# Performance work log

Measured on AMD Instinct MI355X. Metric: run time of the kernel, lower is better.

The kernel has to match this reference:

```python
import jax, jax.numpy as jnp
import numpy as np

N_NODES = 50000
N_EDGES = 600000
D = 128
NEG_SLOPE = 0.2


def _gat_conv(x, src, dst, W, a_src, a_dst, b):
    # x: [N, D]; src/dst: [E'] (self-loops included); PyG GATConv, heads=1
    h = x @ W                               # [N, D]
    alpha_s = h @ a_src                     # [N]
    alpha_d = h @ a_dst                     # [N]
    e = alpha_s[src] + alpha_d[dst]         # [E'] raw scores per edge j->i
    e = jnp.where(e > 0, e, NEG_SLOPE * e)  # LeakyReLU(0.2)
    # segment softmax over incoming edges of each dst node
    m = jax.ops.segment_max(e, dst, num_segments=N_NODES)
    ex = jnp.exp(e - m[dst])
    denom = jax.ops.segment_sum(ex, dst, num_segments=N_NODES)
    alpha = ex / denom[dst]                 # [E']
    out = jax.ops.segment_sum(alpha[:, None] * h[src], dst, num_segments=N_NODES)
    return out + b


def setup_inputs() -> dict:
    key = jax.random.key(0)
    ks = jax.random.split(key, 10)
    scale = 1.0 / np.sqrt(D)
    x = jax.random.normal(ks[0], (N_NODES, D), dtype=jnp.float32)
    edge_index = jax.random.randint(ks[1], (2, N_EDGES), 0, N_NODES, dtype=jnp.int64)
    params = {}
    for i, base in ((1, 2), (2, 6)):
        params[f"W{i}"] = jax.random.normal(ks[base], (D, D), dtype=jnp.float32) * scale
        params[f"a_src{i}"] = jax.random.normal(ks[base + 1], (D,), dtype=jnp.float32) * scale
        params[f"a_dst{i}"] = jax.random.normal(ks[base + 2], (D,), dtype=jnp.float32) * scale
        params[f"b{i}"] = jnp.zeros((D,), dtype=jnp.float32)
    return {"x": x, "edge_index": edge_index, **params}


def reference(x, edge_index, W1, a_src1, a_dst1, b1, W2, a_src2, a_dst2, b2):
    # add self-loops (PyG GATConv default add_self_loops=True)
    loops = jnp.arange(N_NODES, dtype=edge_index.dtype)
    src = jnp.concatenate([edge_index[0], loops])
    dst = jnp.concatenate([edge_index[1], loops])
    h = _gat_conv(x, src, dst, W1, a_src1, a_dst1, b1)
    h = jax.nn.relu(h)  # BasicGNN act between layers, none after last
    out = _gat_conv(h, src, dst, W2, a_src2, a_dst2, b2)
    return out
```

## Files before the change

### kernel.cpp

```cpp
#include <hip/hip_runtime.h>
#include <hip/hip_bf16.h>

#define D 128
#define NEG_SLOPE 0.2f
#define AGG_CHUNK 128
#define CHUNKB 4096

typedef short bf16x8 __attribute__((ext_vector_type(8)));
typedef unsigned short ushort8 __attribute__((ext_vector_type(8)));
typedef float f32x4 __attribute__((ext_vector_type(4)));

__device__ inline unsigned short bfbits(float f) {
  __hip_bfloat16 b = __float2bfloat16(f);
  return *(unsigned short*)&b;
}

__device__ inline float2 bf2_to_f2(unsigned v) {
  return make_float2(__uint_as_float(v << 16), __uint_as_float(v & 0xffff0000u));
}


template <bool RELU, bool BF16IN>
__device__ __forceinline__ void gemm_body(ushort* Wt, int tile,
                                          const void* __restrict__ in,
                                          const float* __restrict__ W,
                                          const float* __restrict__ a_s,
                                          const float* __restrict__ a_d,
                                          ushort* __restrict__ hb,
                                          float* __restrict__ as_out,
                                          float* __restrict__ ad_out, int N) {
  int tid = threadIdx.x;
  for (int u = tid; u < 2048; u += 256) {
    int kp = u >> 5, cg = u & 31;
    int k = kp * 2;
    float4 w0 = *(const float4*)(W + (size_t)k * D + cg * 4);
    float4 w1 = *(const float4*)(W + (size_t)(k + 1) * D + cg * 4);
    float v0[4] = {w0.x, w0.y, w0.z, w0.w};
    float v1[4] = {w1.x, w1.y, w1.z, w1.w};
    #pragma unroll
    for (int i = 0; i < 4; ++i) {
      int c = cg * 4 + i;
      unsigned word = (unsigned)bfbits(v0[i]) | ((unsigned)bfbits(v1[i]) << 16);
      int byte = c * 256 + ((k * 2) ^ ((c & 7) << 4));
      *(unsigned*)((char*)Wt + byte) = word;
    }
  }
  __syncthreads();

  int wave = tid >> 6, lane = tid & 63;
  int lrow = lane & 15, lgrp = lane >> 4;
  int r0 = tile * 128 + wave * 32;
  int rowA[2];
  rowA[0] = min(r0 + lrow, N - 1);
  rowA[1] = min(r0 + 16 + lrow, N - 1);

  f32x4 acc[2][8];
  #pragma unroll
  for (int t = 0; t < 2; ++t)
    #pragma unroll
    for (int nt = 0; nt < 8; ++nt) acc[t][nt] = (f32x4){0.f, 0.f, 0.f, 0.f};

  #pragma unroll
  for (int ks = 0; ks < 4; ++ks) {
    bf16x8 af[2];
    #pragma unroll
    for (int t = 0; t < 2; ++t) {
      if (BF16IN) {
        const ushort* arow = (const ushort*)in + (size_t)rowA[t] * D;
        ushort8 u = *(const ushort8*)(arow + ks * 32 + lgrp * 8);
        if (RELU) {
          #pragma unroll
          for (int j = 0; j < 8; ++j) u[j] = (u[j] & 0x8000u) ? 0 : u[j];
        }
        #pragma unroll
        for (int j = 0; j < 8; ++j) af[t][j] = (short)u[j];
      } else {
        const float* arow = (const float*)in + (size_t)rowA[t] * D;
        float4 a0 = *(const float4*)(arow + ks * 32 + lgrp * 8);
        float4 a1 = *(const float4*)(arow + ks * 32 + lgrp * 8 + 4);
        if (RELU) {
          a0.x = fmaxf(a0.x, 0.f); a0.y = fmaxf(a0.y, 0.f);
          a0.z = fmaxf(a0.z, 0.f); a0.w = fmaxf(a0.w, 0.f);
          a1.x = fmaxf(a1.x, 0.f); a1.y = fmaxf(a1.y, 0.f);
          a1.w = fmaxf(a1.w, 0.f); a1.z = fmaxf(a1.z, 0.f);
        }
        af[t][0] = (short)bfbits(a0.x); af[t][1] = (short)bfbits(a0.y);
        af[t][2] = (short)bfbits(a0.z); af[t][3] = (short)bfbits(a0.w);
        af[t][4] = (short)bfbits(a1.x); af[t][5] = (short)bfbits(a1.y);
        af[t][6] = (short)bfbits(a1.z); af[t][7] = (short)bfbits(a1.w);
      }
    }
    #pragma unroll
    for (int nt = 0; nt < 8; ++nt) {
      int c = nt * 16 + lrow;
      int kb = (ks * 64 + lgrp * 16) ^ ((c & 7) << 4);
      bf16x8 bfr = *(const bf16x8*)((const char*)Wt + c * 256 + kb);
      acc[0][nt] = __builtin_amdgcn_mfma_f32_16x16x32_bf16(af[0], bfr, acc[0][nt], 0, 0, 0);
      acc[1][nt] = __builtin_amdgcn_mfma_f32_16x16x32_bf16(af[1], bfr, acc[1][nt], 0, 0, 0);
    }
  }

  float ps[2][4] = {{0.f,0.f,0.f,0.f},{0.f,0.f,0.f,0.f}};
  float pd[2][4] = {{0.f,0.f,0.f,0.f},{0.f,0.f,0.f,0.f}};
  #pragma unroll
  for (int nt = 0; nt < 8; ++nt) {
    float asc = a_s[nt * 16 + lrow];
    float adc = a_d[nt * 16 + lrow];
    #pragma unroll
    for (int t = 0; t < 2; ++t) {
      #pragma unroll
      for (int r = 0; r < 4; ++r) {
        float v = acc[t][nt][r];
        ps[t][r] += v * asc;
        pd[t][r] += v * adc;
        int row = r0 + t * 16 + lgrp * 4 + r;
        if (row < N) hb[(size_t)row * D + nt * 16 + lrow] = bfbits(v);
      }
    }
  }
  #pragma unroll
  for (int mk = 1; mk < 16; mk <<= 1) {
    #pragma unroll
    for (int t = 0; t < 2; ++t)
      #pragma unroll
      for (int r = 0; r < 4; ++r) {
        ps[t][r] += __shfl_xor(ps[t][r], mk);
        pd[t][r] += __shfl_xor(pd[t][r], mk);
      }
  }
  if (lrow == 0) {
    #pragma unroll
    for (int t = 0; t < 2; ++t)
      #pragma unroll
      for (int r = 0; r < 4; ++r) {
        int row = r0 + t * 16 + lgrp * 4 + r;
        if (row < N) { as_out[row] = ps[t][r]; ad_out[row] = pd[t][r]; }
      }
  }
}

__global__ __launch_bounds__(256) void count_gemm_kernel(const int* __restrict__ ei,
                                                         int* __restrict__ coarse,
                                                         int E, int total, int nbkt, int nblk,
                                                         const float* __restrict__ in,
                                                         const float* __restrict__ W,
                                                         const float* __restrict__ a_s,
                                                         const float* __restrict__ a_d,
                                                         ushort* __restrict__ hb,
                                                         float* __restrict__ as_out,
                                                         float* __restrict__ ad_out, int N) {
  if ((int)blockIdx.x < nblk) {
    __shared__ int hist[256];
    for (int i = threadIdx.x; i < nbkt; i += 256) hist[i] = 0;
    __syncthreads();
    int base = blockIdx.x * CHUNKB;
    int end = min(base + CHUNKB, total);
    for (int e = base + threadIdx.x; e < end; e += 256) {
      int dst = (e < E) ? ei[E + e] : (e - E);
      atomicAdd(&hist[dst >> 8], 1);
    }
    __syncthreads();
    for (int i = threadIdx.x; i < nbkt; i += 256)
      coarse[(size_t)i * nblk + blockIdx.x] = hist[i];
  } else {
    __shared__ ushort Wt[D * D];
    gemm_body<false, false>(Wt, blockIdx.x - nblk, in, W, a_s, a_d, hb, as_out, ad_out, N);
  }
}

__global__ __launch_bounds__(256) void gemm_bf16_kernel(const ushort* __restrict__ in,
                                                        const float* __restrict__ W,
                                                        const float* __restrict__ a_s,
                                                        const float* __restrict__ a_d,
                                                        ushort* __restrict__ hb,
                                                        float* __restrict__ as_out,
                                                        float* __restrict__ ad_out, int N) {
  __shared__ ushort Wt[D * D];
  gemm_body<true, true>(Wt, blockIdx.x, in, W, a_s, a_d, hb, as_out, ad_out, N);
}


__global__ __launch_bounds__(256) void scan_all_kernel(const int* __restrict__ in,
                                                       int* __restrict__ out, int n) {
  __shared__ int wsA[4];
  __shared__ int wsB[4];
  int b = blockIdx.x;
  int tid = threadIdx.x;
  int lane = tid & 63, wid = tid >> 6;

  int pre = 0;
  for (int q = tid; q < b * 256; q += 256) {
    int4 v = *(const int4*)(in + (size_t)q * 4);
    pre += v.x + v.y + v.z + v.w;
  }
  #pragma unroll
  for (int off = 32; off; off >>= 1) pre += __shfl_xor(pre, off);
  if (lane == 0) wsA[wid] = pre;
  __syncthreads();
  int base = wsA[0] + wsA[1] + wsA[2] + wsA[3];

  int i = b * 1024 + tid * 4;
  int4 v = make_int4(0, 0, 0, 0);
  if (i + 3 < n) v = *(const int4*)(in + i);
  else {
    if (i < n) v.x = in[i];
    if (i + 1 < n) v.y = in[i + 1];
    if (i + 2 < n) v.z = in[i + 2];
    if (i + 3 < n) v.w = in[i + 3];
  }
  int s = v.x + v.y + v.z + v.w;
  int incl = s;
  #pragma unroll
  for (int off = 1; off < 64; off <<= 1) {
    int t = __shfl_up(incl, off);
    if (lane >= off) incl += t;
  }
  if (lane == 63) wsB[wid] = incl;
  __syncthreads();
  int wpref = 0;
  #pragma unroll
  for (int w = 0; w < 4; ++w) wpref += (w < wid) ? wsB[w] : 0;
  int run = base + wpref + incl - s;
  if (i < n)     { out[i] = run;     run += v.x; if (i + 1 == n) out[n] = run; }
  if (i + 1 < n) { out[i + 1] = run; run += v.y; if (i + 2 == n) out[n] = run; }
  if (i + 2 < n) { out[i + 2] = run; run += v.z; if (i + 3 == n) out[n] = run; }
  if (i + 3 < n) { out[i + 3] = run; run += v.w; if (i + 4 == n) out[n] = run; }
}

__global__ __launch_bounds__(256) void bucket_scatter_kernel(const int* __restrict__ ei,
                                                             const int* __restrict__ scanout,
                                                             int* __restrict__ stage,
                                                             int E, int total, int nbkt, int nblk) {
  __shared__ int cur[256];
  for (int i = threadIdx.x; i < nbkt; i += 256)
    cur[i] = scanout[(size_t)i * nblk + blockIdx.x];
  __syncthreads();
  int base = blockIdx.x * CHUNKB;
  int end = min(base + CHUNKB, total);
  for (int e = base + threadIdx.x; e < end; e += 256) {
    int src, dst;
    if (e < E) { src = ei[e]; dst = ei[E + e]; }
    else       { src = dst = e - E; }
    int pos = atomicAdd(&cur[dst >> 8], 1);
    stage[pos] = src | (dst << 16);
  }
}

__global__ __launch_bounds__(256) void fine_sort_kernel(const int* __restrict__ stage,
                                                        const int* __restrict__ scanout,
                                                        unsigned* __restrict__ csr,
                                                        int* __restrict__ rowptr,
                                                        int N, int nblk) {
  __shared__ int cnt[256];
  __shared__ int ofs[256];
  __shared__ int wsum[4];
  int b = blockIdx.x;
  int tid = threadIdx.x;
  int rbase = scanout[(size_t)b * nblk];
  int rend = scanout[(size_t)(b + 1) * nblk];
  cnt[tid] = 0;
  __syncthreads();
  for (int e = rbase + tid; e < rend; e += 256)
    atomicAdd(&cnt[((unsigned)stage[e] >> 16) & 255u], 1);
  __syncthreads();
  int v = cnt[tid];
  int lane = tid & 63, wid = tid >> 6;
  int incl = v;
  #pragma unroll
  for (int off = 1; off < 64; off <<= 1) {
    int t = __shfl_up(incl, off);
    if (lane >= off) incl += t;
  }
  if (lane == 63) wsum[wid] = incl;
  __syncthreads();
  int wpref = 0;
  #pragma unroll
  for (int w = 0; w < 4; ++w) wpref += (w < wid) ? wsum[w] : 0;
  int excl = wpref + incl - v;
  ofs[tid] = excl;
  cnt[tid] = 0;
  int n = b * 256 + tid;
  if (n < N) rowptr[n] = rbase + excl;
  if (b == gridDim.x - 1 && tid == 0) rowptr[N] = rend;
  __syncthreads();
  for (int e = rbase + tid; e < rend; e += 256) {
    unsigned p = (unsigned)stage[e];
    int j = (int)((p >> 16) & 255u);
    int pos = rbase + ofs[j] + atomicAdd(&cnt[j], 1);
    csr[pos] = p;
  }
}


template <typename TOUT>
__global__ __launch_bounds__(256) void agg_kernel(const ushort* __restrict__ hb,
                                                  const int* __restrict__ rowptr,
                                                  const unsigned* __restrict__ csr,
                                                  const float* __restrict__ as_,
                                                  const float* __restrict__ ad_,
                                                  const float* __restrict__ bias,
                                                  TOUT* __restrict__ out, int N) {
  int wid = threadIdx.x >> 6;
  int lane = threadIdx.x & 63;
  int n = blockIdx.x * 4 + wid;
  if (n >= N) return;
  int start = rowptr[n], end = rowptr[n + 1];
  int deg = end - start;
  float adv = ad_[n];
  int g = lane >> 4;
  int fl = lane & 15;

  float accf[8] = {0.f, 0.f, 0.f, 0.f, 0.f, 0.f, 0.f, 0.f};
  float denom;

  if (deg <= 32) {
    int s0 = 0;
    float asv = 0.f;
    if (lane < deg) {
      s0 = (int)(csr[start + lane] & 0xffffu);
      asv = as_[s0];
    }
    uint4 pv[8];
    #pragma unroll
    for (int it = 0; it < 8; ++it) {
      int idx = it * 4 + g;
      int sv = __shfl(s0, idx < 64 ? idx : 0);
      if (idx < deg)
        pv[it] = *(const uint4*)(hb + (size_t)sv * D + fl * 8);
    }
    float w0 = 0.f;
    if (lane < deg) {
      float sc = asv + adv;
      sc = sc > 0.f ? sc : NEG_SLOPE * sc;
      w0 = __expf(sc);
    }
    denom = w0;
    #pragma unroll
    for (int off = 32; off; off >>= 1) denom += __shfl_xor(denom, off);
    #pragma unroll
    for (int it = 0; it < 8; ++it) {
      int idx = it * 4 + g;
      float wv = __shfl(w0, idx < 64 ? idx : 0);
      if (idx < deg) {
        float2 f0 = bf2_to_f2(pv[it].x), f1 = bf2_to_f2(pv[it].y);
        float2 f2 = bf2_to_f2(pv[it].z), f3 = bf2_to_f2(pv[it].w);
        accf[0] += wv * f0.x; accf[1] += wv * f0.y;
        accf[2] += wv * f1.x; accf[3] += wv * f1.y;
        accf[4] += wv * f2.x; accf[5] += wv * f2.y;
        accf[6] += wv * f3.x; accf[7] += wv * f3.y;
      }
    }
  } else {
    float wsum = 0.f;
    for (int cbase = start; cbase < end; cbase += AGG_CHUNK) {
      int cend = min(cbase + AGG_CHUNK, end);
      int cnt = cend - cbase;
      int e0 = cbase + lane, e1 = e0 + 64;
      int s0 = 0, s1 = 0;
      float w0 = 0.f, w1 = 0.f;
      if (e0 < cend) {
        s0 = (int)(csr[e0] & 0xffffu);
        float sc = as_[s0] + adv;
        sc = sc > 0.f ? sc : NEG_SLOPE * sc;
        w0 = __expf(sc);
      }
      if (e1 < cend) {
        s1 = (int)(csr[e1] & 0xffffu);
        float sc = as_[s1] + adv;
        sc = sc > 0.f ? sc : NEG_SLOPE * sc;
        w1 = __expf(sc);
      }
      wsum += w0 + w1;
      for (int i = 0; i < cnt; i += 4) {
        int idx = i + g;
        int   sv = (idx < 64) ? __shfl(s0, idx) : __shfl(s1, idx - 64);
        float wv = (idx < 64) ? __shfl(w0, idx) : __shfl(w1, idx - 64);
        uint4 hv = *(const uint4*)(hb + (size_t)sv * D + fl * 8);
        float2 f0 = bf2_to_f2(hv.x), f1 = bf2_to_f2(hv.y);
        float2 f2 = bf2_to_f2(hv.z), f3 = bf2_to_f2(hv.w);
        accf[0] += wv * f0.x; accf[1] += wv * f0.y;
        accf[2] += wv * f1.x; accf[3] += wv * f1.y;
        accf[4] += wv * f2.x; accf[5] += wv * f2.y;
        accf[6] += wv * f3.x; accf[7] += wv * f3.y;
      }
    }
    denom = wsum;
    #pragma unroll
    for (int off = 32; off; off >>= 1) denom += __shfl_xor(denom, off);
  }

  #pragma unroll
  for (int j = 0; j < 8; ++j) accf[j] += __shfl_xor(accf[j], 16);
  #pragma unroll
  for (int j = 0; j < 8; ++j) accf[j] += __shfl_xor(accf[j], 32);

  if (g == 0) {
    float inv = 1.f / denom;
    float4 b0 = *(const float4*)(bias + fl * 8);
    float4 b1 = *(const float4*)(bias + fl * 8 + 4);
    float o[8] = {accf[0] * inv + b0.x, accf[1] * inv + b0.y,
                  accf[2] * inv + b0.z, accf[3] * inv + b0.w,
                  accf[4] * inv + b1.x, accf[5] * inv + b1.y,
                  accf[6] * inv + b1.z, accf[7] * inv + b1.w};
    if (sizeof(TOUT) == 4) {
      float* op = (float*)out + (size_t)n * D + fl * 8;
      *(float4*)op = make_float4(o[0], o[1], o[2], o[3]);
      *(float4*)(op + 4) = make_float4(o[4], o[5], o[6], o[7]);
    } else {
      ushort8 u;
      #pragma unroll
      for (int j = 0; j < 8; ++j) u[j] = bfbits(o[j]);
      *(ushort8*)((ushort*)out + (size_t)n * D + fl * 8) = u;
    }
  }
}


extern "C" void kernel_launch(void* const* d_in, const int* in_sizes, int n_in,
                              void* d_out, int out_size, void* d_ws, size_t ws_size,
                              hipStream_t stream) {
  const float* x   = (const float*)d_in[0];
  const int*   ei  = (const int*)d_in[1];
  const float* W1  = (const float*)d_in[2];
  const float* as1 = (const float*)d_in[3];
  const float* ad1 = (const float*)d_in[4];
  const float* b1  = (const float*)d_in[5];
  const float* W2  = (const float*)d_in[6];
  const float* as2 = (const float*)d_in[7];
  const float* ad2 = (const float*)d_in[8];
  const float* b2  = (const float*)d_in[9];

  int N = in_sizes[0] / D;
  int E = in_sizes[1] / 2;
  int total = E + N;
  int nbkt = (N + 255) >> 8;
  int nblk = (total + CHUNKB - 1) / CHUNKB;
  int nscan = nbkt * nblk;
  int nsb = (nscan + 1023) / 1024;
  int nbG = (N + 127) / 128;

  char* ws = (char*)d_ws;
  size_t off = 0;
  auto alloc = [&](size_t bytes) {
    void* p = ws + off;
    off = (off + bytes + 255) & ~(size_t)255;
    return p;
  };
  ushort*   hb      = (ushort*)alloc((size_t)N * D * sizeof(ushort));
  ushort*   tmpb    = (ushort*)alloc((size_t)N * D * sizeof(ushort));
  float*    alpha_s = (float*)alloc((size_t)N * sizeof(float));
  float*    alpha_d = (float*)alloc((size_t)N * sizeof(float));
  int*      rowptr  = (int*)alloc((size_t)(N + 1) * sizeof(int));
  int*      coarse  = (int*)alloc(((size_t)nscan + 4) * sizeof(int));
  int*      scanout = (int*)alloc((size_t)(nscan + 1) * sizeof(int));
  int*      stage   = (int*)alloc((size_t)total * sizeof(int));
  unsigned* csr     = (unsigned*)alloc((size_t)total * sizeof(unsigned));

  count_gemm_kernel<<<nblk + nbG, 256, 0, stream>>>(ei, coarse, E, total, nbkt, nblk,
                                                    x, W1, as1, ad1, hb, alpha_s, alpha_d, N);
  scan_all_kernel<<<nsb, 256, 0, stream>>>(coarse, scanout, nscan);
  bucket_scatter_kernel<<<nblk, 256, 0, stream>>>(ei, scanout, stage, E, total, nbkt, nblk);
  fine_sort_kernel<<<nbkt, 256, 0, stream>>>(stage, scanout, csr, rowptr, N, nblk);

  agg_kernel<ushort><<<(N + 3) / 4, 256, 0, stream>>>(hb, rowptr, csr, alpha_s, alpha_d,
                                                      b1, tmpb, N);

  gemm_bf16_kernel<<<nbG, 256, 0, stream>>>(tmpb, W2, as2, ad2, hb, alpha_s, alpha_d, N);
  agg_kernel<float><<<(N + 3) / 4, 256, 0, stream>>>(hb, rowptr, csr, alpha_s, alpha_d,
                                                     b2, (float*)d_out, N);
}
```

Before: 120.9 us.

## Fuse scan into scatter/sort kernels and split layer-1 GEMM across three launches

Removes the separate scan kernel. The scatter and sort kernels now compute their own bucket offsets by reducing coarse histogram rows and doing an in-block prefix scan. The layer-1 GEMM tiles are split into thirds, and each third rides along with the count, scatter, or sort kernel so the GEMM overlaps the CSR build stages. This saves one launch, but every block now repeats the coarse-row reductions, and shared memory usage grows to the GEMM's size in the sort and scatter blocks.

```diff
diff --git a/kernel.cpp b/kernel.cpp
--- a/kernel.cpp
+++ b/kernel.cpp
@@ -82,7 +82,7 @@
           a0.x = fmaxf(a0.x, 0.f); a0.y = fmaxf(a0.y, 0.f);
           a0.z = fmaxf(a0.z, 0.f); a0.w = fmaxf(a0.w, 0.f);
           a1.x = fmaxf(a1.x, 0.f); a1.y = fmaxf(a1.y, 0.f);
-          a1.w = fmaxf(a1.w, 0.f); a1.z = fmaxf(a1.z, 0.f);
+          a1.z = fmaxf(a1.z, 0.f); a1.w = fmaxf(a1.w, 0.f);
         }
         af[t][0] = (short)bfbits(a0.x); af[t][1] = (short)bfbits(a0.y);
         af[t][2] = (short)bfbits(a0.z); af[t][3] = (short)bfbits(a0.w);
@@ -138,6 +138,7 @@
       }
   }
 }
+
 
 __global__ __launch_bounds__(256) void count_gemm_kernel(const int* __restrict__ ei,
                                                          int* __restrict__ coarse,
@@ -168,6 +169,143 @@
   }
 }
 
+
+__global__ __launch_bounds__(256) void scatter_gemm_kernel(const int* __restrict__ ei,
+                                                           const int* __restrict__ coarse,
+                                                           int* __restrict__ stage,
+                                                           int E, int total, int nbkt, int nblk,
+                                                           int tile0,
+                                                           const float* __restrict__ in,
+                                                           const float* __restrict__ W,
+                                                           const float* __restrict__ a_s,
+                                                           const float* __restrict__ a_d,
+                                                           ushort* __restrict__ hb,
+                                                           float* __restrict__ as_out,
+                                                           float* __restrict__ ad_out, int N) {
+  __shared__ ushort smem[D * D];
+  if ((int)blockIdx.x < nblk) {
+    int* cur = (int*)smem;
+    int* ws  = (int*)smem + 256;
+    int tid = threadIdx.x;
+    int j = blockIdx.x;
+    int rowtot = 0, cpre = 0;
+    if (tid < nbkt) {
+      const int* row = coarse + (size_t)tid * nblk;
+      for (int q = 0; q < nblk; ++q) {
+        int v = row[q];
+        rowtot += v;
+        cpre += (q < j) ? v : 0;
+      }
+    }
+    int lane = tid & 63, wid = tid >> 6;
+    int incl = rowtot;
+    #pragma unroll
+    for (int off = 1; off < 64; off <<= 1) {
+      int t = __shfl_up(incl, off);
+      if (lane >= off) incl += t;
+    }
+    if (lane == 63) ws[wid] = incl;
+    __syncthreads();
+    int wpref = 0;
+    #pragma unroll
+    for (int w = 0; w < 4; ++w) wpref += (w < wid) ? ws[w] : 0;
+    cur[tid] = wpref + incl - rowtot + cpre;
+    __syncthreads();
+    int base = j * CHUNKB;
+    int end = min(base + CHUNKB, total);
+    for (int e = base + tid; e < end; e += 256) {
+      int src, dst;
+      if (e < E) { src = ei[e]; dst = ei[E + e]; }
+      else       { src = dst = e - E; }
+      int pos = atomicAdd(&cur[dst >> 8], 1);
+      stage[pos] = src | (dst << 16);
+    }
+  } else {
+    gemm_body<false, false>(smem, tile0 + (int)blockIdx.x - nblk, in, W, a_s, a_d,
+                            hb, as_out, ad_out, N);
+  }
+}
+
+
+__global__ __launch_bounds__(256) void sort_gemm_kernel(const int* __restrict__ stage,
+                                                        const int* __restrict__ coarse,
+                                                        unsigned* __restrict__ csr,
+                                                        int* __restrict__ rowptr,
+                                                        int N, int nbkt, int nblk, int tile0,
+                                                        const float* __restrict__ in,
+                                                        const float* __restrict__ W,
+                                                        const float* __restrict__ a_s,
+                                                        const float* __restrict__ a_d,
+                                                        ushort* __restrict__ hb,
+                                                        float* __restrict__ as_out,
+                                                        float* __restrict__ ad_out, int NN) {
+  __shared__ ushort smem[D * D];
+  if ((int)blockIdx.x < nbkt) {
+    int* cnt = (int*)smem;
+    int* ofs = (int*)smem + 256;
+    int* ws  = (int*)smem + 512;
+    int* rr  = (int*)smem + 516;
+    int tid = threadIdx.x;
+    int b = blockIdx.x;
+    int rowtot = 0;
+    if (tid < nbkt) {
+      const int* row = coarse + (size_t)tid * nblk;
+      for (int q = 0; q < nblk; ++q) rowtot += row[q];
+    }
+    int lane = tid & 63, wid = tid >> 6;
+    int incl = rowtot;
+    #pragma unroll
+    for (int off = 1; off < 64; off <<= 1) {
+      int t = __shfl_up(incl, off);
+      if (lane >= off) incl += t;
+    }
+    if (lane == 63) ws[wid] = incl;
+    __syncthreads();
+    int wpref = 0;
+    #pragma unroll
+    for (int w = 0; w < 4; ++w) wpref += (w < wid) ? ws[w] : 0;
+    int Rt = wpref + incl - rowtot;
+    if (tid == b) { rr[0] = Rt; rr[1] = Rt + rowtot; }
+    __syncthreads();
+    int rbase = rr[0], rend = rr[1];
+
+    cnt[tid] = 0;
+    __syncthreads();
+    for (int e = rbase + tid; e < rend; e += 256)
+      atomicAdd(&cnt[((unsigned)stage[e] >> 16) & 255u], 1);
+    __syncthreads();
+    int v = cnt[tid];
+    int incl2 = v;
+    #pragma unroll
+    for (int off = 1; off < 64; off <<= 1) {
+      int t = __shfl_up(incl2, off);
+      if (lane >= off) incl2 += t;
+    }
+    if (lane == 63) ws[wid] = incl2;
+    __syncthreads();
+    int wpref2 = 0;
+    #pragma unroll
+    for (int w = 0; w < 4; ++w) wpref2 += (w < wid) ? ws[w] : 0;
+    int excl = wpref2 + incl2 - v;
+    ofs[tid] = excl;
+    cnt[tid] = 0;
+    int n = b * 256 + tid;
+    if (n < N) rowptr[n] = rbase + excl;
+    if (b == nbkt - 1 && tid == 0) rowptr[N] = rend;
+    __syncthreads();
+    for (int e = rbase + tid; e < rend; e += 256) {
+      unsigned p = (unsigned)stage[e];
+      int j = (int)((p >> 16) & 255u);
+      int pos = rbase + ofs[j] + atomicAdd(&cnt[j], 1);
+      csr[pos] = p;
+    }
+  } else {
+    gemm_body<false, false>(smem, tile0 + (int)blockIdx.x - nbkt, in, W, a_s, a_d,
+                            hb, as_out, ad_out, NN);
+  }
+}
+
+
 __global__ __launch_bounds__(256) void gemm_bf16_kernel(const ushort* __restrict__ in,
                                                         const float* __restrict__ W,
                                                         const float* __restrict__ a_s,
@@ -177,118 +315,6 @@
                                                         float* __restrict__ ad_out, int N) {
   __shared__ ushort Wt[D * D];
   gemm_body<true, true>(Wt, blockIdx.x, in, W, a_s, a_d, hb, as_out, ad_out, N);
-}
-
-
-__global__ __launch_bounds__(256) void scan_all_kernel(const int* __restrict__ in,
-                                                       int* __restrict__ out, int n) {
-  __shared__ int wsA[4];
-  __shared__ int wsB[4];
-  int b = blockIdx.x;
-  int tid = threadIdx.x;
-  int lane = tid & 63, wid = tid >> 6;
-
-  int pre = 0;
-  for (int q = tid; q < b * 256; q += 256) {
-    int4 v = *(const int4*)(in + (size_t)q * 4);
-    pre += v.x + v.y + v.z + v.w;
-  }
-  #pragma unroll
-  for (int off = 32; off; off >>= 1) pre += __shfl_xor(pre, off);
-  if (lane == 0) wsA[wid] = pre;
-  __syncthreads();
-  int base = wsA[0] + wsA[1] + wsA[2] + wsA[3];
-
-  int i = b * 1024 + tid * 4;
-  int4 v = make_int4(0, 0, 0, 0);
-  if (i + 3 < n) v = *(const int4*)(in + i);
-  else {
-    if (i < n) v.x = in[i];
-    if (i + 1 < n) v.y = in[i + 1];
-    if (i + 2 < n) v.z = in[i + 2];
-    if (i + 3 < n) v.w = in[i + 3];
-  }
-  int s = v.x + v.y + v.z + v.w;
-  int incl = s;
-  #pragma unroll
-  for (int off = 1; off < 64; off <<= 1) {
-    int t = __shfl_up(incl, off);
-    if (lane >= off) incl += t;
-  }
-  if (lane == 63) wsB[wid] = incl;
-  __syncthreads();
-  int wpref = 0;
-  #pragma unroll
-  for (int w = 0; w < 4; ++w) wpref += (w < wid) ? wsB[w] : 0;
-  int run = base + wpref + incl - s;
-  if (i < n)     { out[i] = run;     run += v.x; if (i + 1 == n) out[n] = run; }
-  if (i + 1 < n) { out[i + 1] = run; run += v.y; if (i + 2 == n) out[n] = run; }
-  if (i + 2 < n) { out[i + 2] = run; run += v.z; if (i + 3 == n) out[n] = run; }
-  if (i + 3 < n) { out[i + 3] = run; run += v.w; if (i + 4 == n) out[n] = run; }
-}
-
-__global__ __launch_bounds__(256) void bucket_scatter_kernel(const int* __restrict__ ei,
-                                                             const int* __restrict__ scanout,
-                                                             int* __restrict__ stage,
-                                                             int E, int total, int nbkt, int nblk) {
-  __shared__ int cur[256];
-  for (int i = threadIdx.x; i < nbkt; i += 256)
-    cur[i] = scanout[(size_t)i * nblk + blockIdx.x];
-  __syncthreads();
-  int base = blockIdx.x * CHUNKB;
-  int end = min(base + CHUNKB, total);
-  for (int e = base + threadIdx.x; e < end; e += 256) {
-    int src, dst;
-    if (e < E) { src = ei[e]; dst = ei[E + e]; }
-    else       { src = dst = e - E; }
-    int pos = atomicAdd(&cur[dst >> 8], 1);
-    stage[pos] = src | (dst << 16);
-  }
-}
-
-__global__ __launch_bounds__(256) void fine_sort_kernel(const int* __restrict__ stage,
-                                                        const int* __restrict__ scanout,
-                                                        unsigned* __restrict__ csr,
-                                                        int* __restrict__ rowptr,
-                                                        int N, int nblk) {
-  __shared__ int cnt[256];
-  __shared__ int ofs[256];
-  __shared__ int wsum[4];
-  int b = blockIdx.x;
-  int tid = threadIdx.x;
-  int rbase = scanout[(size_t)b * nblk];
-  int rend = scanout[(size_t)(b + 1) * nblk];
-  cnt[tid] = 0;
-  __syncthreads();
-  for (int e = rbase + tid; e < rend; e += 256)
-    atomicAdd(&cnt[((unsigned)stage[e] >> 16) & 255u], 1);
-  __syncthreads();
-  int v = cnt[tid];
-  int lane = tid & 63, wid = tid >> 6;
-  int incl = v;
-  #pragma unroll
-  for (int off = 1; off < 64; off <<= 1) {
-    int t = __shfl_up(incl, off);
-    if (lane >= off) incl += t;
-  }
-  if (lane == 63) wsum[wid] = incl;
-  __syncthreads();
-  int wpref = 0;
-  #pragma unroll
-  for (int w = 0; w < 4; ++w) wpref += (w < wid) ? wsum[w] : 0;
-  int excl = wpref + incl - v;
-  ofs[tid] = excl;
-  cnt[tid] = 0;
-  int n = b * 256 + tid;
-  if (n < N) rowptr[n] = rbase + excl;
-  if (b == gridDim.x - 1 && tid == 0) rowptr[N] = rend;
-  __syncthreads();
-  for (int e = rbase + tid; e < rend; e += 256) {
-    unsigned p = (unsigned)stage[e];
-    int j = (int)((p >> 16) & 255u);
-    int pos = rbase + ofs[j] + atomicAdd(&cnt[j], 1);
-    csr[pos] = p;
-  }
 }
 
 
@@ -436,8 +462,10 @@
   int nbkt = (N + 255) >> 8;
   int nblk = (total + CHUNKB - 1) / CHUNKB;
   int nscan = nbkt * nblk;
-  int nsb = (nscan + 1023) / 1024;
   int nbG = (N + 127) / 128;
+  int G_A = nbG / 3;
+  int G_B = nbG / 3;
+  int G_C = nbG - G_A - G_B;
 
   char* ws = (char*)d_ws;
   size_t off = 0;
@@ -452,15 +480,18 @@
   float*    alpha_d = (float*)alloc((size_t)N * sizeof(float));
   int*      rowptr  = (int*)alloc((size_t)(N + 1) * sizeof(int));
   int*      coarse  = (int*)alloc(((size_t)nscan + 4) * sizeof(int));
-  int*      scanout = (int*)alloc((size_t)(nscan + 1) * sizeof(int));
   int*      stage   = (int*)alloc((size_t)total * sizeof(int));
   unsigned* csr     = (unsigned*)alloc((size_t)total * sizeof(unsigned));
 
-  count_gemm_kernel<<<nblk + nbG, 256, 0, stream>>>(ei, coarse, E, total, nbkt, nblk,
+  count_gemm_kernel<<<nblk + G_A, 256, 0, stream>>>(ei, coarse, E, total, nbkt, nblk,
                                                     x, W1, as1, ad1, hb, alpha_s, alpha_d, N);
-  scan_all_kernel<<<nsb, 256, 0, stream>>>(coarse, scanout, nscan);
-  bucket_scatter_kernel<<<nblk, 256, 0, stream>>>(ei, scanout, stage, E, total, nbkt, nblk);
-  fine_sort_kernel<<<nbkt, 256, 0, stream>>>(stage, scanout, csr, rowptr, N, nblk);
+  scatter_gemm_kernel<<<nblk + G_B, 256, 0, stream>>>(ei, coarse, stage, E, total, nbkt, nblk,
+                                                      G_A, x, W1, as1, ad1, hb,
+                                                      alpha_s, alpha_d, N);
+  sort_gemm_kernel<<<nbkt + G_C, 256, 0, stream>>>(stage, coarse, csr, rowptr,
+                                                   N, nbkt, nblk, G_A + G_B,
+                                                   x, W1, as1, ad1, hb,
+                                                   alpha_s, alpha_d, N);
 
   agg_kernel<ushort><<<(N + 3) / 4, 256, 0, stream>>>(hb, rowptr, csr, alpha_s, alpha_d,
                                                       b1, tmpb, N);
```

Result: slower. 140.8 us (+16.4%).
